# Optimization experiments

Measured on AMD Instinct MI355X. Metric: run time of the kernel, lower is better.

The kernel has to match this reference:

```python
import jax, jax.numpy as jnp
import numpy as np

EMBED_DIM = 1024
NUM_HEADS = 16
HEAD_DIM = EMBED_DIM // NUM_HEADS
B, S = 4, 2048


def setup_inputs() -> dict:
    key = jax.random.key(0)
    k1, k2, k3, k4, k5 = jax.random.split(key, 5)
    x = jax.random.normal(k1, (B, S, EMBED_DIM), dtype=jnp.float32)
    # torch nn.Linear params: W [out, in], b [out]; init scale ~ 1/sqrt(in)
    s = 1.0 / np.sqrt(EMBED_DIM)
    qkv_w = jax.random.uniform(k2, (3 * EMBED_DIM, EMBED_DIM), jnp.float32, -s, s)
    qkv_b = jax.random.uniform(k3, (3 * EMBED_DIM,), jnp.float32, -s, s)
    out_w = jax.random.uniform(k4, (EMBED_DIM, EMBED_DIM), jnp.float32, -s, s)
    out_b = jax.random.uniform(k5, (EMBED_DIM,), jnp.float32, -s, s)
    return {"x": x, "qkv_w": qkv_w, "qkv_b": qkv_b, "out_w": out_w, "out_b": out_b}


def reference(x, qkv_w, qkv_b, out_w, out_b):
    b, s, e = x.shape
    # qkv: [B,S,3E]
    qkv = x @ qkv_w.T + qkv_b
    # Faithful to source: reshape to [B,S,H,3*hd] then transpose -> [B,H,S,3*hd]
    qkv = qkv.reshape(b, s, NUM_HEADS, 3 * HEAD_DIM).transpose(0, 2, 1, 3)
    q, k, v = jnp.split(qkv, 3, axis=-1)  # each [B,H,S,hd]
    q = q / np.sqrt(HEAD_DIM).astype(np.float32)
    scores = jnp.einsum('bhqd,bhkd->bhqk', q, k)  # [B,H,S,S]
    attn = jax.nn.softmax(scores, axis=-1)
    out = jnp.einsum('bhqk,bhkd->bhqd', attn, v)  # [B,H,S,hd]
    out = out.transpose(0, 2, 1, 3).reshape(b, s, e)
    return out @ out_w.T + out_b
```

## Files before the change

### kernel.cpp

```cpp
#include <hip/hip_runtime.h>

#define EMBED   1024
#define THREE_E 3072
#define NHEAD   16
#define HDIM    64
#define BATCH   4
#define SEQ     2048
#define MTOK    (BATCH * SEQ)
#define QKW     2048

typedef __attribute__((ext_vector_type(8)))  _Float16 half8;
typedef __attribute__((ext_vector_type(4)))  _Float16 half4;
typedef __attribute__((ext_vector_type(4)))  float    f32x4;
typedef __attribute__((ext_vector_type(4)))  unsigned uint4v;

#define QSCALE 0.18033688011112042f

__device__ inline f32x4 mfma16(half8 a, half8 b, f32x4 c) {
    return __builtin_amdgcn_mfma_f32_16x16x32_f16(a, b, c, 0, 0, 0);
}

__device__ inline float exp2x(float x) {
    float r;
    asm("v_exp_f32 %0, %1" : "=v"(r) : "v"(x));
    return r;
}
__device__ inline unsigned pk2(float a, float b) {
    return __builtin_bit_cast(unsigned, __builtin_amdgcn_cvt_pkrtz(a, b));
}

__device__ inline void gld16(const void* g, void* l) {
    __builtin_amdgcn_global_load_lds(
        (const __attribute__((address_space(1))) unsigned*)g,
        (__attribute__((address_space(3))) unsigned*)l, 16, 0, 0);
}

__global__ __launch_bounds__(256) void tohi3_kernel(
    const float* __restrict__ x,  _Float16* __restrict__ xo,
    const float* __restrict__ w1, _Float16* __restrict__ w1o,
    const float* __restrict__ w2, _Float16* __restrict__ w2o)
{
    const int bid = blockIdx.x;
    const float* src; _Float16* dst; int base;
    if (bid < 8192)             { src = x;  dst = xo;  base = bid * 1024; }
    else if (bid < 8192 + 3072) { src = w1; dst = w1o; base = (bid - 8192) * 1024; }
    else                        { src = w2; dst = w2o; base = (bid - 11264) * 1024; }
    const int i = base + (threadIdx.x << 2);
    const float4 v = *(const float4*)(src + i);
    half4 h;
    h[0] = (_Float16)v.x; h[1] = (_Float16)v.y;
    h[2] = (_Float16)v.z; h[3] = (_Float16)v.w;
    *(half4*)(dst + i) = h;
}

template<int OMODE>
__global__ __launch_bounds__(512, 2) void gemm_big(
    const _Float16* __restrict__ Ahi,
    const _Float16* __restrict__ Bhi,
    const float*  __restrict__ bias,
    float* __restrict__ Cf,
    _Float16* __restrict__ QKhi,
    _Float16* __restrict__ Vthi,
    int N, int K)
{
    __shared__ __align__(16) _Float16 sA[3][8][2][64][8];
    __shared__ __align__(16) _Float16 sB[3][16][2][64][8];

    const int tid  = threadIdx.x;
    const int w    = tid >> 6;
    const int lane = tid & 63;
    const int quad = lane >> 4;
    const int c    = lane & 15;
    const int wr   = w >> 2, wc = w & 3;

    const int gx   = gridDim.x;
    const int nwg  = gx * gridDim.y;
    const int lin0 = blockIdx.y * gx + blockIdx.x;
    const int wg   = (lin0 & 7) * (nwg >> 3) + (lin0 >> 3);
    const int m0   = (wg / gx) << 7;
    const int n0   = (wg % gx) << 8;

    f32x4 acc[4][4];
#pragma unroll
    for (int i = 0; i < 4; ++i)
#pragma unroll
        for (int j = 0; j < 4; ++j) acc[i][j] = (f32x4){0.f, 0.f, 0.f, 0.f};

    const int rg0 = w >> 1, ksb = w & 1;
    const size_t sK64 = (size_t)64 * K;
    const _Float16* ap = Ahi + (size_t)(m0 + rg0 * 16 + c) * K + ksb * 32 + quad * 8;
    const _Float16* bp = Bhi + (size_t)(n0 + rg0 * 16 + c) * K + ksb * 32 + quad * 8;

    auto stage_p0 = [&](int sl) {
        gld16(ap,            &sA[sl][rg0][ksb][0][0]);
        gld16(ap + sK64,     &sA[sl][4 + rg0][ksb][0][0]);
        gld16(bp,            &sB[sl][rg0][ksb][0][0]);
    };
    auto stage_p1 = [&](int sl) {
        gld16(bp + sK64,     &sB[sl][4 + rg0][ksb][0][0]);
        gld16(bp + 2 * sK64, &sB[sl][8 + rg0][ksb][0][0]);
        gld16(bp + 3 * sK64, &sB[sl][12 + rg0][ksb][0][0]);
        ap += 64; bp += 64;
    };

    stage_p0(0); stage_p1(0);
    stage_p0(1); stage_p1(1);

    const int NT = K >> 6;
    int slot = 0;
    for (int t = 0; t < NT; ++t) {
        if (t + 1 < NT) { asm volatile("s_waitcnt vmcnt(6)" ::: "memory"); }
        else            { asm volatile("s_waitcnt vmcnt(0)" ::: "memory"); }
        __builtin_amdgcn_s_barrier();

        const bool pre = (t + 2) < NT;
        int ns = slot + 2; if (ns >= 3) ns -= 3;

        half8 aH[4][2], bH[4][2];
#pragma unroll
        for (int fr = 0; fr < 4; ++fr)
#pragma unroll
            for (int ks = 0; ks < 2; ++ks)
                aH[fr][ks] = *(const half8*)&sA[slot][wr * 4 + fr][ks][lane][0];
#pragma unroll
        for (int fc = 0; fc < 2; ++fc)
#pragma unroll
            for (int ks = 0; ks < 2; ++ks)
                bH[fc][ks] = *(const half8*)&sB[slot][wc * 4 + fc][ks][lane][0];
        if (pre) stage_p0(ns);
        __builtin_amdgcn_s_setprio(1);
#pragma unroll
        for (int fr = 0; fr < 4; ++fr)
#pragma unroll
            for (int fc = 0; fc < 2; ++fc)
#pragma unroll
                for (int ks = 0; ks < 2; ++ks)
                    acc[fr][fc] = mfma16(aH[fr][ks], bH[fc][ks], acc[fr][fc]);
        __builtin_amdgcn_s_setprio(0);
        __builtin_amdgcn_s_barrier();

#pragma unroll
        for (int fc = 2; fc < 4; ++fc)
#pragma unroll
            for (int ks = 0; ks < 2; ++ks)
                bH[fc][ks] = *(const half8*)&sB[slot][wc * 4 + fc][ks][lane][0];
        if (pre) stage_p1(ns);
        __builtin_amdgcn_s_setprio(1);
#pragma unroll
        for (int fr = 0; fr < 4; ++fr)
#pragma unroll
            for (int fc = 2; fc < 4; ++fc)
#pragma unroll
                for (int ks = 0; ks < 2; ++ks)
                    acc[fr][fc] = mfma16(aH[fr][ks], bH[fc][ks], acc[fr][fc]);
        __builtin_amdgcn_s_setprio(0);

        slot = (slot == 2) ? 0 : slot + 1;
    }

#pragma unroll
    for (int fc = 0; fc < 4; ++fc) {
        const int n  = n0 + wc * 64 + fc * 16 + c;
        const float bb = bias[n];
        const int h  = n / 192;
        const int rem = n - h * 192;
#pragma unroll
        for (int fr = 0; fr < 4; ++fr) {
            const int mb = m0 + wr * 64 + fr * 16 + (quad << 2);
            if constexpr (OMODE == 0) {
#pragma unroll
                for (int r = 0; r < 4; ++r)
                    Cf[(size_t)(mb + r) * N + n] = acc[fr][fc][r] + bb;
            } else {
                if (rem < 128) {
                    const size_t col = h * 128 + rem;
                    const float scale = (rem < 64) ? QSCALE : 1.0f;
#pragma unroll
                    for (int r = 0; r < 4; ++r)
                        QKhi[(size_t)(mb + r) * QKW + col] =
                            (_Float16)((acc[fr][fc][r] + bb) * scale);
                } else {
                    const int d = rem - 128;
                    const int b = mb >> 11;
                    const int s = mb & 2047;
                    half4 h4;
#pragma unroll
                    for (int r = 0; r < 4; ++r)
                        h4[r] = (_Float16)(acc[fr][fc][r] + bb);
                    const size_t off = ((size_t)(h * 64 + d) * BATCH + b) * SEQ + s;
                    *(half4*)(Vthi + off) = h4;
                }
            }
        }
    }
}

__global__ __launch_bounds__(256, 4) void attn_mfma(
    const _Float16* __restrict__ qkhi,
    const _Float16* __restrict__ vthi,
    _Float16* __restrict__ attnf)
{
    __shared__ __align__(16) _Float16 Kf[2][8][512];
    __shared__ __align__(16) _Float16 Vf[2][8][512];

    const int tid  = threadIdx.x;
    const int w    = tid >> 6;
    const int lane = tid & 63;
    const int quad = lane >> 4;
    const int c    = lane & 15;

    const int lin = blockIdx.x;
    const int g   = lin & 7;
    const int s   = lin >> 3;
    const int bh  = g * 8 + (s >> 4);
    const int qt  = s & 15;
    const int b   = bh >> 4, h = bh & 15;
    const int q0  = qt * 128;

    const size_t bSEQ  = (size_t)b * SEQ;
    const int    qcol  = h * 128;
    const int    kcol  = h * 128 + 64;
    const size_t vbase = ((size_t)(h * 64) * BATCH + b) * SEQ;

    half8 qh[2][2];
#pragma unroll
    for (int t = 0; t < 2; ++t) {
        const size_t row = (bSEQ + q0 + w * 32 + t * 16 + c) * QKW;
#pragma unroll
        for (int ks = 0; ks < 2; ++ks)
            qh[t][ks] = *(const half8*)(qkhi + row + qcol + ks * 32 + quad * 8);
    }

    float lrun[2] = {0.f, 0.f};
    f32x4 oacc[4][2];
#pragma unroll
    for (int t = 0; t < 2; ++t)
#pragma unroll
        for (int v = 0; v < 4; ++v) oacc[v][t] = (f32x4){0.f, 0.f, 0.f, 0.f};

    const int ku0 = w >> 1,       kks0 = w & 1;
    const int ku1 = (4 + w) >> 1, kks1 = (4 + w) & 1;
    const _Float16* kp0 = qkhi + (bSEQ + ku0 * 16 + c) * QKW + kcol + kks0 * 32 + quad * 8;
    const _Float16* kp1 = qkhi + (bSEQ + ku1 * 16 + c) * QKW + kcol + kks1 * 32 + quad * 8;
    const int lswz = lane ^ ((((lane >> 3) & 1) << 1) | (((lane >> 4) & 1) << 2));
    const int qs   = lswz >> 4, cs = lswz & 15;
    const _Float16* vp0 = vthi + vbase + (size_t)(ku0 * 16 + cs) * (BATCH * SEQ) + kks0 * 32 + qs * 8;
    const _Float16* vp1 = vthi + vbase + (size_t)(ku1 * 16 + cs) * (BATCH * SEQ) + kks1 * 32 + qs * 8;

    auto stageKV = [&](int bfs) {
        gld16(kp0, &Kf[bfs][w][0]);
        gld16(kp1, &Kf[bfs][4 + w][0]);
        gld16(vp0, &Vf[bfs][w][0]);
        gld16(vp1, &Vf[bfs][4 + w][0]);
        kp0 += 64 * QKW; kp1 += 64 * QKW; vp0 += 64; vp1 += 64;
    };

    stageKV(0);
    int bf = 0;

    for (int kt = 0; kt < SEQ / 64; ++kt) {
        __syncthreads();
        if (kt + 1 < SEQ / 64) stageKV(bf ^ 1);

        f32x4 sacc[2][4];
        __builtin_amdgcn_s_setprio(1);
#pragma unroll
        for (int u = 0; u < 4; ++u) {
            const half8 kh0 = *(const half8*)&Kf[bf][(u << 1) + 0][lane << 3];
            const half8 kh1 = *(const half8*)&Kf[bf][(u << 1) + 1][lane << 3];
#pragma unroll
            for (int t = 0; t < 2; ++t) {
                f32x4 a = (f32x4){0.f, 0.f, 0.f, 0.f};
                a = mfma16(kh0, qh[t][0], a);
                a = mfma16(kh1, qh[t][1], a);
                sacc[t][u] = a;
            }
        }
        __builtin_amdgcn_s_setprio(0);

        half8 pb[2][2];
#pragma unroll
        for (int t = 0; t < 2; ++t) {
            float rs = 0.f;
#pragma unroll
            for (int gp = 0; gp < 2; ++gp) {
                uint4v wd;
#pragma unroll
                for (int hf = 0; hf < 2; ++hf) {
                    const int u = 2 * gp + hf;
                    const float p0 = exp2x(sacc[t][u][0]);
                    const float p1 = exp2x(sacc[t][u][1]);
                    const float p2 = exp2x(sacc[t][u][2]);
                    const float p3 = exp2x(sacc[t][u][3]);
                    rs += (p0 + p1) + (p2 + p3);
                    if (hf == 0) { wd.x = pk2(p0, p1); wd.y = pk2(p2, p3); }
                    else         { wd.z = pk2(p0, p1); wd.w = pk2(p2, p3); }
                }
                pb[t][gp] = __builtin_bit_cast(half8, wd);
            }
            lrun[t] += rs;
        }

        half8 vb[4][2];
        {
            const int qp0 = quad >> 1;
            const int qp1 = 2 + (quad >> 1);
            int e0 = ((qp0 << 4) + c) * 8 + ((quad & 1) << 2);
            int e1 = ((qp1 << 4) + c) * 8 + ((quad & 1) << 2);
            e0 ^= (((c >> 3) & 1) << 4) ^ ((qp0 & 1) << 5);
            e1 ^= (((c >> 3) & 1) << 4) ^ ((qp1 & 1) << 5);
#pragma unroll
            for (int v = 0; v < 4; ++v)
#pragma unroll
                for (int gp = 0; gp < 2; ++gp) {
                    const half4 a0 = *(const half4*)&Vf[bf][(v << 1) + gp][e0];
                    const half4 a1 = *(const half4*)&Vf[bf][(v << 1) + gp][e1];
                    half8 vv;
#pragma unroll
                    for (int i = 0; i < 4; ++i) { vv[i] = a0[i]; vv[4 + i] = a1[i]; }
                    vb[v][gp] = vv;
                }
        }

        __builtin_amdgcn_s_setprio(1);
#pragma unroll
        for (int t = 0; t < 2; ++t)
#pragma unroll
            for (int v = 0; v < 4; ++v) {
                f32x4 a = oacc[v][t];
                a = mfma16(vb[v][0], pb[t][0], a);
                a = mfma16(vb[v][1], pb[t][1], a);
                oacc[v][t] = a;
            }
        __builtin_amdgcn_s_setprio(0);

        bf ^= 1;
    }

#pragma unroll
    for (int t = 0; t < 2; ++t) {
        float lr = lrun[t];
        lr += __shfl_xor(lr, 16);
        lr += __shfl_xor(lr, 32);
        const float inv = 1.0f / lr;
        const int tok = q0 + w * 32 + t * 16 + c;
#pragma unroll
        for (int v = 0; v < 4; ++v) {
            half4 o;
#pragma unroll
            for (int r = 0; r < 4; ++r) o[r] = (_Float16)(oacc[v][t][r] * inv);
            *(half4*)&attnf[(bSEQ + tok) * EMBED + h * HDIM + v * 16 + (quad << 2)] = o;
        }
    }
}

extern "C" void kernel_launch(void* const* d_in, const int* in_sizes, int n_in,
                              void* d_out, int out_size, void* d_ws, size_t ws_size,
                              hipStream_t stream)
{
    const float* x     = (const float*)d_in[0];
    const float* qkv_w = (const float*)d_in[1];
    const float* qkv_b = (const float*)d_in[2];
    const float* out_w = (const float*)d_in[3];
    const float* out_b = (const float*)d_in[4];

    _Float16* qkhi  = (_Float16*)d_ws;
    _Float16* vthi  = qkhi  + (size_t)MTOK * QKW;
    _Float16* w1hi  = vthi  + (size_t)NHEAD * HDIM * BATCH * SEQ;
    _Float16* w2hi  = w1hi  + (size_t)THREE_E * EMBED;
    _Float16* attnf = w2hi  + (size_t)EMBED * EMBED;

    _Float16* xhi = (_Float16*)d_out;

    tohi3_kernel<<<dim3(12288), 256, 0, stream>>>(x, xhi, qkv_w, w1hi, out_w, w2hi);

    gemm_big<1><<<dim3(THREE_E / 256, MTOK / 128), 512, 0, stream>>>(
        xhi, w1hi, qkv_b, nullptr, qkhi, vthi, THREE_E, EMBED);

    attn_mfma<<<dim3(1024), 256, 0, stream>>>(qkhi, vthi, attnf);

    gemm_big<0><<<dim3(EMBED / 256, MTOK / 128), 512, 0, stream>>>(
        attnf, w2hi, out_b, (float*)d_out, nullptr, nullptr, EMBED, EMBED);
}
```

Baseline: 289.5 us.

## Pre-tile V into MFMA fragment layout and compute row sums via MFMA

The QKV projection epilogue now writes V into a per-(head,batch,64-key tile) layout that already matches the MFMA B-operand fragment order. The attention kernel can then stage V with contiguous loads and read each fragment with a single half8 LDS load, replacing the swizzled half4 gathers. The softmax row sum is also moved from VALU adds plus cross-lane shuffles onto extra MFMAs against a ones vector. This cuts VALU and LDS work per tile, but the projection epilogue now does scattered half4 stores and each tile issues more MFMA instructions.

```diff
diff --git a/kernel.cpp b/kernel.cpp
--- a/kernel.cpp
+++ b/kernel.cpp
@@ -180,14 +180,24 @@
                         QKhi[(size_t)(mb + r) * QKW + col] =
                             (_Float16)((acc[fr][fc][r] + bb) * scale);
                 } else {
-                    const int d = rem - 128;
-                    const int b = mb >> 11;
-                    const int s = mb & 2047;
+                    const int d  = rem - 128;
+                    const int b  = mb >> 11;
+                    const int s  = mb & 2047;
+                    const int kt = s >> 6;
+                    const int rs = s & 63;
+                    const int gp = rs >> 5;
+                    const int hf = (rs >> 4) & 1;
+                    const int kq = (rs >> 2) & 3;
+                    const int v  = d >> 4;
+                    const int cl = d & 15;
                     half4 h4;
 #pragma unroll
                     for (int r = 0; r < 4; ++r)
                         h4[r] = (_Float16)(acc[fr][fc][r] + bb);
-                    const size_t off = ((size_t)(h * 64 + d) * BATCH + b) * SEQ + s;
+                    const size_t off =
+                        ((((size_t)(h * BATCH + b) * (SEQ / 64) + kt) * 8
+                          + (v * 2 + gp)) * 512)
+                        + (size_t)(kq * 16 + cl) * 8 + hf * 4;
                     *(half4*)(Vthi + off) = h4;
                 }
             }
@@ -220,7 +230,6 @@
     const size_t bSEQ  = (size_t)b * SEQ;
     const int    qcol  = h * 128;
     const int    kcol  = h * 128 + 64;
-    const size_t vbase = ((size_t)(h * 64) * BATCH + b) * SEQ;
 
     half8 qh[2][2];
 #pragma unroll
@@ -231,28 +240,32 @@
             qh[t][ks] = *(const half8*)(qkhi + row + qcol + ks * 32 + quad * 8);
     }
 
-    float lrun[2] = {0.f, 0.f};
+    f32x4 lacc[2];
     f32x4 oacc[4][2];
 #pragma unroll
-    for (int t = 0; t < 2; ++t)
+    for (int t = 0; t < 2; ++t) {
+        lacc[t] = (f32x4){0.f, 0.f, 0.f, 0.f};
 #pragma unroll
         for (int v = 0; v < 4; ++v) oacc[v][t] = (f32x4){0.f, 0.f, 0.f, 0.f};
+    }
+
+    const half8 one8 = {(_Float16)1.f, (_Float16)1.f, (_Float16)1.f, (_Float16)1.f,
+                        (_Float16)1.f, (_Float16)1.f, (_Float16)1.f, (_Float16)1.f};
 
     const int ku0 = w >> 1,       kks0 = w & 1;
     const int ku1 = (4 + w) >> 1, kks1 = (4 + w) & 1;
     const _Float16* kp0 = qkhi + (bSEQ + ku0 * 16 + c) * QKW + kcol + kks0 * 32 + quad * 8;
     const _Float16* kp1 = qkhi + (bSEQ + ku1 * 16 + c) * QKW + kcol + kks1 * 32 + quad * 8;
-    const int lswz = lane ^ ((((lane >> 3) & 1) << 1) | (((lane >> 4) & 1) << 2));
-    const int qs   = lswz >> 4, cs = lswz & 15;
-    const _Float16* vp0 = vthi + vbase + (size_t)(ku0 * 16 + cs) * (BATCH * SEQ) + kks0 * 32 + qs * 8;
-    const _Float16* vp1 = vthi + vbase + (size_t)(ku1 * 16 + cs) * (BATCH * SEQ) + kks1 * 32 + qs * 8;
+    const _Float16* vp0 = vthi + ((size_t)(h * BATCH + b) * (SEQ / 64)) * 4096
+                               + (size_t)w * 512 + lane * 8;
+    const _Float16* vp1 = vp0 + 4 * 512;
 
     auto stageKV = [&](int bfs) {
         gld16(kp0, &Kf[bfs][w][0]);
         gld16(kp1, &Kf[bfs][4 + w][0]);
         gld16(vp0, &Vf[bfs][w][0]);
         gld16(vp1, &Vf[bfs][4 + w][0]);
-        kp0 += 64 * QKW; kp1 += 64 * QKW; vp0 += 64; vp1 += 64;
+        kp0 += 64 * QKW; kp1 += 64 * QKW; vp0 += 4096; vp1 += 4096;
     };
 
     stageKV(0);
@@ -280,8 +293,7 @@
 
         half8 pb[2][2];
 #pragma unroll
-        for (int t = 0; t < 2; ++t) {
-            float rs = 0.f;
+        for (int t = 0; t < 2; ++t)
 #pragma unroll
             for (int gp = 0; gp < 2; ++gp) {
                 uint4v wd;
@@ -292,39 +304,22 @@
                     const float p1 = exp2x(sacc[t][u][1]);
                     const float p2 = exp2x(sacc[t][u][2]);
                     const float p3 = exp2x(sacc[t][u][3]);
-                    rs += (p0 + p1) + (p2 + p3);
                     if (hf == 0) { wd.x = pk2(p0, p1); wd.y = pk2(p2, p3); }
                     else         { wd.z = pk2(p0, p1); wd.w = pk2(p2, p3); }
                 }
                 pb[t][gp] = __builtin_bit_cast(half8, wd);
             }
-            lrun[t] += rs;
-        }
 
         half8 vb[4][2];
-        {
-            const int qp0 = quad >> 1;
-            const int qp1 = 2 + (quad >> 1);
-            int e0 = ((qp0 << 4) + c) * 8 + ((quad & 1) << 2);
-            int e1 = ((qp1 << 4) + c) * 8 + ((quad & 1) << 2);
-            e0 ^= (((c >> 3) & 1) << 4) ^ ((qp0 & 1) << 5);
-            e1 ^= (((c >> 3) & 1) << 4) ^ ((qp1 & 1) << 5);
-#pragma unroll
-            for (int v = 0; v < 4; ++v)
-#pragma unroll
-                for (int gp = 0; gp < 2; ++gp) {
-                    const half4 a0 = *(const half4*)&Vf[bf][(v << 1) + gp][e0];
-                    const half4 a1 = *(const half4*)&Vf[bf][(v << 1) + gp][e1];
-                    half8 vv;
-#pragma unroll
-                    for (int i = 0; i < 4; ++i) { vv[i] = a0[i]; vv[4 + i] = a1[i]; }
-                    vb[v][gp] = vv;
-                }
-        }
+#pragma unroll
+        for (int v = 0; v < 4; ++v)
+#pragma unroll
+            for (int gp = 0; gp < 2; ++gp)
+                vb[v][gp] = *(const half8*)&Vf[bf][(v << 1) + gp][lane << 3];
 
         __builtin_amdgcn_s_setprio(1);
 #pragma unroll
-        for (int t = 0; t < 2; ++t)
+        for (int t = 0; t < 2; ++t) {
 #pragma unroll
             for (int v = 0; v < 4; ++v) {
                 f32x4 a = oacc[v][t];
@@ -332,6 +327,11 @@
                 a = mfma16(vb[v][1], pb[t][1], a);
                 oacc[v][t] = a;
             }
+            f32x4 l = lacc[t];
+            l = mfma16(one8, pb[t][0], l);
+            l = mfma16(one8, pb[t][1], l);
+            lacc[t] = l;
+        }
         __builtin_amdgcn_s_setprio(0);
 
         bf ^= 1;
@@ -339,10 +339,7 @@
 
 #pragma unroll
     for (int t = 0; t < 2; ++t) {
-        float lr = lrun[t];
-        lr += __shfl_xor(lr, 16);
-        lr += __shfl_xor(lr, 32);
-        const float inv = 1.0f / lr;
+        const float inv = 1.0f / lacc[t][0];
         const int tok = q0 + w * 32 + t * 16 + c;
 #pragma unroll
         for (int v = 0; v < 4; ++v) {
```

Measured after the change: 276.2 us. 1.05x faster.
